# Kernel tuning notes

Measured on AMD Instinct MI355X. Metric: run time of the kernel, lower is better.

The kernel has to match this reference:

```python
import jax, jax.numpy as jnp
import numpy as np

NUM_CATEGORIES = 64
INPUT_DIM = 256
HIDDEN_DIM = 256
N = 4096  # number of samples (each with its own category)
M = 16    # rows per sample


def setup_inputs() -> dict:
    key = jax.random.key(0)
    k_x, k_cat, k_W = jax.random.split(key, 3)
    x = jax.random.normal(k_x, (N, M, INPUT_DIM), dtype=jnp.float32)
    cat_ids = jax.random.randint(k_cat, (N,), 0, NUM_CATEGORIES, dtype=jnp.int64)
    W = 0.02 * jax.random.normal(k_W, (NUM_CATEGORIES, INPUT_DIM, HIDDEN_DIM), dtype=jnp.float32)
    b = jnp.zeros((NUM_CATEGORIES, HIDDEN_DIM), dtype=jnp.float32)
    return {"x": x, "cat_ids": cat_ids, "W": W, "b": b}


def reference(x, cat_ids, W, b):
    # Gather per-sample weights/biases, then batched matmul + bias add.
    selected_W = W[cat_ids]              # [N, input_dim, hidden_dim]
    selected_b = b[cat_ids]              # [N, hidden_dim]
    out = jnp.einsum('nmi,nih->nmh', x, selected_W) + selected_b[:, None, :]
    return out
```

## Files before the change

### kernel.cpp

```cpp
#include <hip/hip_runtime.h>
#include <hip/hip_bf16.h>
#include <stdint.h>

#define N_SAMPLES 4096
#define M_ROWS 16
#define K_DIM 256
#define H_DIM 256
#define N_CATS 64
#define SPB 4
#define MAX_PADDED (N_SAMPLES + N_CATS * (SPB - 1))
#define NGROUP (MAX_PADDED / SPB)
#define GPX (NGROUP / 8)
#define GEMM_GRID (NGROUP * 2)
#define AROW 264

typedef _Float16 half8 __attribute__((ext_vector_type(8)));
typedef _Float16 half4 __attribute__((ext_vector_type(4)));
typedef float floatx4 __attribute__((ext_vector_type(4)));

#define WT_BYTES ((size_t)N_CATS * K_DIM * H_DIM * 2)
#define GCAT_OFF WT_BYTES
#define ORD_OFF  (WT_BYTES + 4288)
#define WS_NEED  (ORD_OFF + (size_t)MAX_PADDED * 4)

__global__ __launch_bounds__(256)
void prep_combined(const float* __restrict__ W, _Float16* __restrict__ Wt,
                   const int* __restrict__ cat, int* __restrict__ ord,
                   int* __restrict__ gcat) {
  const int tid = threadIdx.x;
  if (blockIdx.x < 1024) {
    __shared__ _Float16 t[64][72];
    const int bid = blockIdx.x;
    const int c  = bid >> 4;
    const int kb = (bid >> 2) & 3;
    const int hb = bid & 3;
    const int r  = tid >> 2;
    const int cg = (tid & 3) * 16;
    const float* src = W + ((size_t)c << 16) + (size_t)(kb * 64 + r) * 256 + hb * 64 + cg;
#pragma unroll
    for (int j = 0; j < 16; j += 4) {
      float4 v = *(const float4*)(src + j);
      t[r][cg + j + 0] = (_Float16)v.x;
      t[r][cg + j + 1] = (_Float16)v.y;
      t[r][cg + j + 2] = (_Float16)v.z;
      t[r][cg + j + 3] = (_Float16)v.w;
    }
    __syncthreads();
    _Float16* dst = Wt + ((size_t)c << 16) + (size_t)(hb * 64 + r) * 256 + kb * 64 + cg;
    half8 o0, o1;
#pragma unroll
    for (int j = 0; j < 8; j++) o0[j] = t[cg + j][r];
#pragma unroll
    for (int j = 0; j < 8; j++) o1[j] = t[cg + 8 + j][r];
    *(half8*)(dst) = o0;
    *(half8*)(dst + 8) = o1;
  } else {
    __shared__ int hist[N_CATS];
    __shared__ int poffs[N_CATS];
    __shared__ int curs[N_CATS];
    if (tid < N_CATS) hist[tid] = 0;
    for (int i = tid; i < MAX_PADDED; i += 256) ord[i] = -1;
    for (int i = tid; i < NGROUP; i += 256) gcat[i] = 0;
    __syncthreads();
    for (int i = tid; i < N_SAMPLES; i += 256) atomicAdd(&hist[cat[i]], 1);
    __syncthreads();
    if (tid == 0) {
      int run = 0;
      for (int c = 0; c < N_CATS; c++) {
        poffs[c] = run;
        run += ((hist[c] + SPB - 1) / SPB) * SPB;
      }
    }
    if (tid < N_CATS) curs[tid] = 0;
    __syncthreads();
    if (tid < N_CATS) {
      const int c = tid;
      const int g0 = poffs[c] >> 2;
      const int ng = (hist[c] + SPB - 1) >> 2;
      for (int g = 0; g < ng; g++) gcat[g0 + g] = c;
    }
    for (int i = tid; i < N_SAMPLES; i += 256) {
      int c = cat[i];
      int p = poffs[c] + atomicAdd(&curs[c], 1);
      ord[p] = i;
    }
  }
}

__global__ __launch_bounds__(256, 3)
void gemm_kernel(const float* __restrict__ x, const float* __restrict__ bias,
                 const _Float16* __restrict__ Wt, const int* __restrict__ ord,
                 const int* __restrict__ gcat, float* __restrict__ out) {
  __shared__ __align__(16) _Float16 sA[64 * AROW];

  const int tid = threadIdx.x;
  const int B = blockIdx.x;
  const int xcd = B & 7;
  const int slot = B >> 3;
  const int h_half = slot & 1;
  const int group = xcd * GPX + (slot >> 1);
  const int h0 = h_half << 7;

  const int cat = gcat[group];
  const int4 sm = *(const int4*)(ord + group * 4);
  if (sm.x < 0) return;

  const int wid  = tid >> 6;
  const int lane = tid & 63;
  const int l15  = lane & 15;
  const int quad = lane >> 4;

  const _Float16* wb = Wt + ((size_t)cat << 16) +
                       (size_t)(h0 + wid * 32 + l15) * K_DIM + quad * 8;

  half8 bf[5][2];
#pragma unroll
  for (int kt = 0; kt < 4; kt++) {
    bf[kt][0] = *(const half8*)(wb + kt * 32);
    bf[kt][1] = *(const half8*)(wb + 16 * K_DIM + kt * 32);
  }
  const float bv0 = bias[cat * H_DIM + h0 + wid * 32 + l15];
  const float bv1 = bias[cat * H_DIM + h0 + wid * 32 + 16 + l15];
  __builtin_amdgcn_sched_barrier(0);

  const int smp = (wid == 0) ? sm.x : (wid == 1) ? sm.y : (wid == 2) ? sm.z : sm.w;
  const float* asrc = (smp >= 0) ? (x + ((size_t)smp << 12)) : nullptr;
  _Float16* adst = sA + (size_t)(wid * 16) * AROW;
  if (asrc) {
#pragma unroll
    for (int j = 0; j < 16; j++) {
      float4 v = *(const float4*)(asrc + j * 256 + lane * 4);
      half4 h;
      h[0] = (_Float16)v.x; h[1] = (_Float16)v.y;
      h[2] = (_Float16)v.z; h[3] = (_Float16)v.w;
      *(half4*)(adst + (size_t)j * AROW + lane * 4) = h;
    }
  } else {
    half4 h;
#pragma unroll
    for (int e = 0; e < 4; e++) h[e] = (_Float16)0.0f;
#pragma unroll
    for (int j = 0; j < 16; j++)
      *(half4*)(adst + (size_t)j * AROW + lane * 4) = h;
  }

  floatx4 acc[4][2];
#pragma unroll
  for (int i = 0; i < 4; i++)
#pragma unroll
    for (int j = 0; j < 2; j++)
#pragma unroll
      for (int e = 0; e < 4; e++) acc[i][j][e] = 0.0f;

  __syncthreads();

#pragma unroll
  for (int kt = 0; kt < 8; kt++) {
    if (kt < 4) {
      bf[(kt + 4) % 5][0] = *(const half8*)(wb + (kt + 4) * 32);
      bf[(kt + 4) % 5][1] = *(const half8*)(wb + 16 * K_DIM + (kt + 4) * 32);
      __builtin_amdgcn_sched_barrier(0);
    }
    half8 af[4];
#pragma unroll
    for (int mt = 0; mt < 4; mt++)
      af[mt] = *(const half8*)&sA[(size_t)(mt * 16 + l15) * AROW + kt * 32 + quad * 8];
#pragma unroll
    for (int mt = 0; mt < 4; mt++) {
      acc[mt][0] = __builtin_amdgcn_mfma_f32_16x16x32_f16(af[mt], bf[kt % 5][0], acc[mt][0], 0, 0, 0);
      acc[mt][1] = __builtin_amdgcn_mfma_f32_16x16x32_f16(af[mt], bf[kt % 5][1], acc[mt][1], 0, 0, 0);
    }
  }

  const int srow[4] = {sm.x, sm.y, sm.z, sm.w};
#pragma unroll
  for (int mt = 0; mt < 4; mt++) {
    const int s = srow[mt];
    if (s < 0) continue;
    float* obase = out + ((size_t)s << 12);
#pragma unroll
    for (int nt = 0; nt < 2; nt++) {
      const int col = h0 + wid * 32 + nt * 16 + l15;
      const float bv = nt ? bv1 : bv0;
#pragma unroll
      for (int rr = 0; rr < 4; rr++) {
        const int row = quad * 4 + rr;
        obase[(size_t)row * H_DIM + col] = acc[mt][nt][rr] + bv;
      }
    }
  }
}

__global__ __launch_bounds__(256)
void naive_kernel(const float* __restrict__ x, const int* __restrict__ cat,
                  const float* __restrict__ W, const float* __restrict__ bias,
                  float* __restrict__ out) {
  __shared__ float sx[16 * 256];
  const int n = blockIdx.x;
  const int tid = threadIdx.x;
  const int c = cat[n];
  const float* xs = x + (size_t)n * 16 * 256;
  for (int i = tid; i < 16 * 256; i += 256) sx[i] = xs[i];
  __syncthreads();
  const float* Wc = W + ((size_t)c << 16);
  float accv[16];
  float bv = bias[c * 256 + tid];
#pragma unroll
  for (int m = 0; m < 16; m++) accv[m] = bv;
  for (int k = 0; k < 256; k++) {
    float w = Wc[(size_t)k * 256 + tid];
#pragma unroll
    for (int m = 0; m < 16; m++) accv[m] += sx[m * 256 + k] * w;
  }
#pragma unroll
  for (int m = 0; m < 16; m++) out[((size_t)n * 16 + m) * 256 + tid] = accv[m];
}

extern "C" void kernel_launch(void* const* d_in, const int* in_sizes, int n_in,
                              void* d_out, int out_size, void* d_ws, size_t ws_size,
                              hipStream_t stream) {
  const float* x    = (const float*)d_in[0];
  const int*   cat  = (const int*)d_in[1];
  const float* W    = (const float*)d_in[2];
  const float* bias = (const float*)d_in[3];
  float* out = (float*)d_out;

  if (ws_size < WS_NEED) {
    naive_kernel<<<N_SAMPLES, 256, 0, stream>>>(x, cat, W, bias, out);
    return;
  }

  char* ws = (char*)d_ws;
  _Float16* Wt = (_Float16*)ws;
  int* gcat = (int*)(ws + GCAT_OFF);
  int* ord  = (int*)(ws + ORD_OFF);

  prep_combined<<<1025, 256, 0, stream>>>(W, Wt, cat, ord, gcat);
  gemm_kernel<<<GEMM_GRID, 256, 0, stream>>>(x, bias, Wt, ord, gcat, out);
}
```

Before: 163.0 us.

## Pre-convert x to swizzled fp16 and stream it to LDS via global_load_lds

Adds a prep pass that converts x to fp16 in an XOR-swizzled layout in workspace. A new gemm kernel then loads A tiles straight into LDS with global_load_lds, which avoids per-thread conversion and padded LDS rows, and raises occupancy to 4 blocks per CU. The cost is an extra full round trip of x through memory (read fp32, write fp16, read again), and the path only runs when the workspace is large enough.

```diff
diff --git a/kernel.cpp b/kernel.cpp
--- a/kernel.cpp
+++ b/kernel.cpp
@@ -18,19 +18,29 @@
 typedef _Float16 half4 __attribute__((ext_vector_type(4)));
 typedef float floatx4 __attribute__((ext_vector_type(4)));
 
-#define WT_BYTES ((size_t)N_CATS * K_DIM * H_DIM * 2)
-#define GCAT_OFF WT_BYTES
-#define ORD_OFF  (WT_BYTES + 4288)
-#define WS_NEED  (ORD_OFF + (size_t)MAX_PADDED * 4)
+#define GLOAD_LDS(g, l)                                          \
+  __builtin_amdgcn_global_load_lds(                              \
+      (const __attribute__((address_space(1))) void*)(g),        \
+      (__attribute__((address_space(3))) void*)(l), 16, 0, 0)
+
+#define WT_BYTES  ((size_t)N_CATS * K_DIM * H_DIM * 2)
+#define X16_BYTES ((size_t)N_SAMPLES * M_ROWS * K_DIM * 2)
+#define GCAT_OFF_F (WT_BYTES + X16_BYTES)
+#define ORD_OFF_F  (GCAT_OFF_F + 4288)
+#define WS_NEED_F  (ORD_OFF_F + (size_t)MAX_PADDED * 4)
+#define GCAT_OFF_S WT_BYTES
+#define ORD_OFF_S  (WT_BYTES + 4288)
+#define WS_NEED_S  (ORD_OFF_S + (size_t)MAX_PADDED * 4)
 
 __global__ __launch_bounds__(256)
 void prep_combined(const float* __restrict__ W, _Float16* __restrict__ Wt,
                    const int* __restrict__ cat, int* __restrict__ ord,
-                   int* __restrict__ gcat) {
+                   int* __restrict__ gcat,
+                   const float* __restrict__ x, _Float16* __restrict__ x16) {
   const int tid = threadIdx.x;
-  if (blockIdx.x < 1024) {
+  const int bid = blockIdx.x;
+  if (bid < 1024) {
     __shared__ _Float16 t[64][72];
-    const int bid = blockIdx.x;
     const int c  = bid >> 4;
     const int kb = (bid >> 2) & 3;
     const int hb = bid & 3;
@@ -54,7 +64,7 @@
     for (int j = 0; j < 8; j++) o1[j] = t[cg + 8 + j][r];
     *(half8*)(dst) = o0;
     *(half8*)(dst + 8) = o1;
-  } else {
+  } else if (bid == 1024) {
     __shared__ int hist[N_CATS];
     __shared__ int poffs[N_CATS];
     __shared__ int curs[N_CATS];
@@ -84,13 +94,120 @@
       int p = poffs[c] + atomicAdd(&curs[c], 1);
       ord[p] = i;
     }
+  } else {
+    const int s = bid - 1025;
+    const float* src = x + ((size_t)s << 12);
+    _Float16* dst = x16 + ((size_t)s << 12);
+#pragma unroll
+    for (int it = 0; it < 4; it++) {
+      const int r = it * 4 + (tid >> 6);
+      const int c = (tid & 63) << 2;
+      float4 v = *(const float4*)(src + r * 256 + c);
+      half4 h;
+      h[0] = (_Float16)v.x; h[1] = (_Float16)v.y;
+      h[2] = (_Float16)v.z; h[3] = (_Float16)v.w;
+      const int slot = c >> 3;
+      *(half4*)(dst + r * 256 + (((slot ^ (r & 7)) << 3) | (c & 7))) = h;
+    }
+  }
+}
+
+__global__ __launch_bounds__(256, 4)
+void gemm_dma(const _Float16* __restrict__ x16, const float* __restrict__ bias,
+              const _Float16* __restrict__ Wt, const int* __restrict__ ord,
+              const int* __restrict__ gcat, float* __restrict__ out) {
+  __shared__ __align__(16) _Float16 sA[64 * 256];
+
+  const int tid = threadIdx.x;
+  const int B = blockIdx.x;
+  const int xcd = B & 7;
+  const int slot = B >> 3;
+  const int h_half = slot & 1;
+  const int group = xcd * GPX + (slot >> 1);
+  const int h0 = h_half << 7;
+
+  const int cat = gcat[group];
+  const int4 sm = *(const int4*)(ord + group * 4);
+  if (sm.x < 0) return;
+
+  const int wid  = tid >> 6;
+  const int lane = tid & 63;
+  const int l15  = lane & 15;
+  const int quad = lane >> 4;
+
+  const _Float16* wb = Wt + ((size_t)cat << 16) +
+                       (size_t)(h0 + wid * 32 + l15) * K_DIM + quad * 8;
+
+  half8 bf[5][2];
+#pragma unroll
+  for (int kt = 0; kt < 4; kt++) {
+    bf[kt][0] = *(const half8*)(wb + kt * 32);
+    bf[kt][1] = *(const half8*)(wb + 16 * K_DIM + kt * 32);
+  }
+  const float bv0 = bias[cat * H_DIM + h0 + wid * 32 + l15];
+  const float bv1 = bias[cat * H_DIM + h0 + wid * 32 + 16 + l15];
+  __builtin_amdgcn_sched_barrier(0);
+
+  const int smp0 = (wid == 0) ? sm.x : (wid == 1) ? sm.y : (wid == 2) ? sm.z : sm.w;
+  const int smp  = (smp0 >= 0) ? smp0 : sm.x;
+  const _Float16* asrc = x16 + ((size_t)smp << 12) + (lane << 3);
+  _Float16* adst = sA + wid * 4096;
+#pragma unroll
+  for (int i = 0; i < 8; i++)
+    GLOAD_LDS(asrc + i * 512, adst + i * 512);
+
+  floatx4 acc[4][2];
+#pragma unroll
+  for (int i = 0; i < 4; i++)
+#pragma unroll
+    for (int j = 0; j < 2; j++)
+#pragma unroll
+      for (int e = 0; e < 4; e++) acc[i][j][e] = 0.0f;
+
+  __syncthreads();
+
+#pragma unroll
+  for (int kt = 0; kt < 8; kt++) {
+    if (kt < 4) {
+      bf[(kt + 4) % 5][0] = *(const half8*)(wb + (kt + 4) * 32);
+      bf[(kt + 4) % 5][1] = *(const half8*)(wb + 16 * K_DIM + (kt + 4) * 32);
+      __builtin_amdgcn_sched_barrier(0);
+    }
+    half8 af[4];
+#pragma unroll
+    for (int mt = 0; mt < 4; mt++)
+      af[mt] = *(const half8*)&sA[(size_t)(mt * 16 + l15) * 256 +
+                                  (((kt * 4 + quad) ^ (l15 & 7)) << 3)];
+#pragma unroll
+    for (int mt = 0; mt < 4; mt++) {
+      acc[mt][0] = __builtin_amdgcn_mfma_f32_16x16x32_f16(af[mt], bf[kt % 5][0], acc[mt][0], 0, 0, 0);
+      acc[mt][1] = __builtin_amdgcn_mfma_f32_16x16x32_f16(af[mt], bf[kt % 5][1], acc[mt][1], 0, 0, 0);
+    }
+  }
+
+  const int srow[4] = {sm.x, sm.y, sm.z, sm.w};
+#pragma unroll
+  for (int mt = 0; mt < 4; mt++) {
+    const int s = srow[mt];
+    if (s < 0) continue;
+    float* obase = out + ((size_t)s << 12);
+#pragma unroll
+    for (int nt = 0; nt < 2; nt++) {
+      const int col = h0 + wid * 32 + nt * 16 + l15;
+      const float bv = nt ? bv1 : bv0;
+#pragma unroll
+      for (int rr = 0; rr < 4; rr++) {
+        const int row = quad * 4 + rr;
+        obase[(size_t)row * H_DIM + col] = acc[mt][nt][rr] + bv;
+      }
+    }
   }
 }
 
 __global__ __launch_bounds__(256, 3)
-void gemm_kernel(const float* __restrict__ x, const float* __restrict__ bias,
-                 const _Float16* __restrict__ Wt, const int* __restrict__ ord,
-                 const int* __restrict__ gcat, float* __restrict__ out) {
+void gemm_small(const float* __restrict__ x, const float* __restrict__ bias,
+                const _Float16* __restrict__ Wt, const int* __restrict__ ord,
+                const int* __restrict__ gcat, float* __restrict__ out) {
   __shared__ __align__(16) _Float16 sA[64 * AROW];
 
   const int tid = threadIdx.x;
@@ -225,16 +342,21 @@
   const float* bias = (const float*)d_in[3];
   float* out = (float*)d_out;
 
-  if (ws_size < WS_NEED) {
+  char* ws = (char*)d_ws;
+  if (ws_size >= WS_NEED_F) {
+    _Float16* Wt  = (_Float16*)ws;
+    _Float16* x16 = (_Float16*)(ws + WT_BYTES);
+    int* gcat = (int*)(ws + GCAT_OFF_F);
+    int* ord  = (int*)(ws + ORD_OFF_F);
+    prep_combined<<<1025 + N_SAMPLES, 256, 0, stream>>>(W, Wt, cat, ord, gcat, x, x16);
+    gemm_dma<<<GEMM_GRID, 256, 0, stream>>>(x16, bias, Wt, ord, gcat, out);
+  } else if (ws_size >= WS_NEED_S) {
+    _Float16* Wt = (_Float16*)ws;
+    int* gcat = (int*)(ws + GCAT_OFF_S);
+    int* ord  = (int*)(ws + ORD_OFF_S);
+    prep_combined<<<1025, 256, 0, stream>>>(W, Wt, cat, ord, gcat, x, nullptr);
+    gemm_small<<<GEMM_GRID, 256, 0, stream>>>(x, bias, Wt, ord, gcat, out);
+  } else {
     naive_kernel<<<N_SAMPLES, 256, 0, stream>>>(x, cat, W, bias, out);
-    return;
-  }
-
-  char* ws = (char*)d_ws;
-  _Float16* Wt = (_Float16*)ws;
-  int* gcat = (int*)(ws + GCAT_OFF);
-  int* ord  = (int*)(ws + ORD_OFF);
-
-  prep_combined<<<1025, 256, 0, stream>>>(W, Wt, cat, ord, gcat);
-  gemm_kernel<<<GEMM_GRID, 256, 0, stream>>>(x, bias, Wt, ord, gcat, out);
-}
+  }
+}
```

New measurement: 159.7 us. 2.1% less time.
